# Kernel tuning notes

Hardware: AMD Instinct MI355X
Metric: run time of the kernel (lower is better)

## Reference

```python
import math
import jax, jax.numpy as jnp
import numpy as np

N = 100000       # nodes
K = 32           # fixed neighbor fanout
D_IN = 128
D_OUT = 128
TPERC = 0.45


def setup_inputs() -> dict:
    key = jax.random.key(0)
    k1, k2, k3 = jax.random.split(key, 3)
    x = jax.random.normal(k1, (N, D_IN), dtype=jnp.float32)
    # nn.Linear weight [out, in], no bias
    W = jax.random.normal(k2, (D_OUT, D_IN), dtype=jnp.float32) * (1.0 / math.sqrt(D_IN))
    nbrs = jax.random.randint(k3, (N, K), 0, N, dtype=jnp.int32)
    return {"x": x, "W": W, "nbrs": nbrs}


def reference(x, W, nbrs):
    # h = Linear(x): [N, D_OUT]
    h = jnp.einsum("nd,od->no", x, W)
    # gather neighbor messages: [N, K, D_OUT]
    msgs = h[nbrs]
    # per-channel sort over the neighbor axis (matches torch.sort(dim=0) per node)
    msgs = jnp.sort(msgs, axis=1)
    remove = math.floor(K * TPERC)  # static: 14
    if remove > 0:
        msgs = msgs[:, remove:K - remove]
    # trimmed mean over remaining neighbors; activation is identity (None)
    return jnp.mean(msgs, axis=1)
```

## Files before the change

kernel.cpp:

```cpp
#include <hip/hip_runtime.h>
#include <hip/hip_fp16.h>

#define NN 100000
#define KK 32
#define DD 128

typedef _Float16 v8h __attribute__((ext_vector_type(8)));
typedef _Float16 v4h __attribute__((ext_vector_type(4)));
typedef _Float16 v2h __attribute__((ext_vector_type(2)));
typedef float    v4f __attribute__((ext_vector_type(4)));

#define LDH 136

__global__ __launch_bounds__(256)
void gemm_mfma_kernel(const float* __restrict__ x, const float* __restrict__ W,
                      _Float16* __restrict__ h) {
    __shared__ _Float16 w_lds[DD * LDH];
    __shared__ _Float16 x_lds[128 * LDH];

    const int tid = threadIdx.x;
    const int block_row = blockIdx.x * 128;

    {
        const float4* ws = (const float4*)W;
        #pragma unroll
        for (int t = 0; t < 16; ++t) {
            const int fi = tid + 256 * t;
            const int r = fi >> 5, c4 = fi & 31;
            const float4 f = ws[fi];
            v4h p = { (_Float16)f.x, (_Float16)f.y, (_Float16)f.z, (_Float16)f.w };
            *(v4h*)&w_lds[r * LDH + c4 * 4] = p;
        }
    }
    {
        const float4* xs = (const float4*)x;
        #pragma unroll
        for (int t = 0; t < 16; ++t) {
            const int fi = tid + 256 * t;
            const int r = fi >> 5, c4 = fi & 31;
            const int gr = block_row + r;
            float4 f = make_float4(0.f, 0.f, 0.f, 0.f);
            if (gr < NN) f = xs[(size_t)gr * 32 + c4];
            v4h p = { (_Float16)f.x, (_Float16)f.y, (_Float16)f.z, (_Float16)f.w };
            *(v4h*)&x_lds[r * LDH + c4 * 4] = p;
        }
    }
    __syncthreads();

    const int wv   = tid >> 6;
    const int lane = tid & 63;
    const int m    = lane & 15;
    const int quad = lane >> 4;

    const v4f zero = {0.f, 0.f, 0.f, 0.f};
    v4f acc[2][8];
    #pragma unroll
    for (int nt = 0; nt < 2; ++nt)
        #pragma unroll
        for (int ot = 0; ot < 8; ++ot) acc[nt][ot] = zero;

    #pragma unroll
    for (int ks = 0; ks < 4; ++ks) {
        const int kb = ks * 32 + quad * 8;
        const v8h xf0 = *(const v8h*)&x_lds[(wv * 32 + m) * LDH + kb];
        const v8h xf1 = *(const v8h*)&x_lds[(wv * 32 + 16 + m) * LDH + kb];
        #pragma unroll
        for (int ot = 0; ot < 8; ++ot) {
            const v8h wf = *(const v8h*)&w_lds[(ot * 16 + m) * LDH + kb];
            acc[0][ot] = __builtin_amdgcn_mfma_f32_16x16x32_f16(wf, xf0, acc[0][ot], 0, 0, 0);
            acc[1][ot] = __builtin_amdgcn_mfma_f32_16x16x32_f16(wf, xf1, acc[1][ot], 0, 0, 0);
        }
    }

    #pragma unroll
    for (int nt = 0; nt < 2; ++nt) {
        const int xr = block_row + wv * 32 + nt * 16 + m;
        if (xr < NN) {
            #pragma unroll
            for (int ot = 0; ot < 8; ++ot) {
                const v4f a = acc[nt][ot];
                v4h p = { (_Float16)a.x, (_Float16)a.y, (_Float16)a.z, (_Float16)a.w };
                *(v4h*)&h[(size_t)xr * DD + ot * 16 + quad * 4] = p;
            }
        }
    }
}

struct CEp { signed char a, b; };
struct Net16 { CEp ce[63]; };

constexpr int oem_merge(CEp* out, int c, int lo, int n, int r) {
    const int m = r * 2;
    if (m < n) {
        c = oem_merge(out, c, lo, n, m);
        c = oem_merge(out, c, lo + r, n, m);
        for (int i = lo + r; i + r < lo + n; i += m) {
            out[c].a = (signed char)i; out[c].b = (signed char)(i + r); ++c;
        }
    } else {
        out[c].a = (signed char)lo; out[c].b = (signed char)(lo + r); ++c;
    }
    return c;
}
constexpr int oem_sort(CEp* out, int c, int lo, int n) {
    if (n > 1) {
        const int m = n / 2;
        c = oem_sort(out, c, lo, m);
        c = oem_sort(out, c, lo + m, m);
        c = oem_merge(out, c, lo, n, 1);
    }
    return c;
}
constexpr Net16 make_net16() {
    Net16 net{};
    (void)oem_sort(net.ce, 0, 0, 16);
    return net;
}
constexpr Net16 NET16 = make_net16();

constexpr int WMAP(int i) { return i < 16 ? i : 47 - i; }

#define PKMIN(d, s0, s1) asm("v_pk_min_f16 %0, %1, %2" : "=v"(d) : "v"(s0), "v"(s1))
#define PKMAX(d, s0, s1) asm("v_pk_max_f16 %0, %1, %2" : "=v"(d) : "v"(s0), "v"(s1))

#define CEW(p, q) do {                                                  \
    v2h na_, xa_, nb_, xb_;                                             \
    PKMIN(na_, va[p], va[q]); PKMAX(xa_, va[p], va[q]);                 \
    PKMIN(nb_, vb[p], vb[q]); PKMAX(xb_, vb[p], vb[q]);                 \
    va[p] = na_; va[q] = xa_; vb[p] = nb_; vb[q] = xb_; } while (0)

__global__ __launch_bounds__(256)
void trimmed_mean_kernel(const _Float16* __restrict__ h, const int* __restrict__ nbrs,
                         float* __restrict__ out) {
    __shared__ int s_nbr[8][KK];

    const int tid = threadIdx.x;
    const int row_base = blockIdx.x * 8;

    s_nbr[tid >> 5][tid & 31] = nbrs[(size_t)row_base * KK + tid];
    __syncthreads();

    const int brow = tid >> 5;
    const int cq   = tid & 31;
    const int row  = row_base + brow;

    const uint2* hq = (const uint2*)h;

    v2h va[KK];
    v2h vb[KK];
    #pragma unroll
    for (int k = 0; k < KK; ++k) {
        const int idx = s_nbr[brow][k];
        const uint2 u = hq[idx * 32 + cq];
        va[k] = __builtin_bit_cast(v2h, u.x);
        vb[k] = __builtin_bit_cast(v2h, u.y);
    }

    #pragma unroll
    for (int t = 0; t < 63; ++t) CEW(NET16.ce[t].a, NET16.ce[t].b);
    #pragma unroll
    for (int t = 0; t < 63; ++t) CEW(NET16.ce[t].a + 16, NET16.ce[t].b + 16);

    #pragma unroll
    for (int i = 0; i < 16; ++i) CEW(WMAP(i), WMAP(i + 16));
    #pragma unroll
    for (int i = 0; i < 8; ++i) { CEW(WMAP(i), WMAP(i + 8));
                                  CEW(WMAP(i + 16), WMAP(i + 24)); }
    #pragma unroll
    for (int i = 8; i < 12; ++i) { CEW(WMAP(i), WMAP(i + 4));
                                   CEW(WMAP(i + 8), WMAP(i + 12)); }
    CEW(WMAP(12), WMAP(14)); CEW(WMAP(13), WMAP(15));
    CEW(WMAP(16), WMAP(18)); CEW(WMAP(17), WMAP(19));

    float4 o;
    o.x = ((float)va[14].x + (float)va[15].x + (float)va[31].x + (float)va[30].x) * 0.25f;
    o.y = ((float)va[14].y + (float)va[15].y + (float)va[31].y + (float)va[30].y) * 0.25f;
    o.z = ((float)vb[14].x + (float)vb[15].x + (float)vb[31].x + (float)vb[30].x) * 0.25f;
    o.w = ((float)vb[14].y + (float)vb[15].y + (float)vb[31].y + (float)vb[30].y) * 0.25f;
    ((float4*)(out + (size_t)row * DD))[cq] = o;
}

extern "C" void kernel_launch(void* const* d_in, const int* in_sizes, int n_in,
                              void* d_out, int out_size, void* d_ws, size_t ws_size,
                              hipStream_t stream) {
    const float* x    = (const float*)d_in[0];
    const float* W    = (const float*)d_in[1];
    const int*   nbrs = (const int*)d_in[2];
    float*       out  = (float*)d_out;
    _Float16*    h    = (_Float16*)d_ws;

    (void)in_sizes; (void)n_in; (void)out_size; (void)ws_size;

    gemm_mfma_kernel<<<(NN + 127) / 128, 256, 0, stream>>>(x, W, h);
    trimmed_mean_kernel<<<NN / 8, 256, 0, stream>>>(h, nbrs, out);
}
```

Measured before the change: 228.6 us.

## Split h into column slices and process one slice per block

The GEMM now writes h in a sliced layout: four column slices of 32 fp16 each, stored as contiguous [NN,32] arrays. The trimmed-mean kernel assigns one slice per block, with 16 rows per block and 16 threads per row. Each thread loads one 32-bit fp16 pair per neighbor instead of two, which halves the register arrays. The aim is better cache locality for the random gathers, since each slice is a smaller working set, and higher occupancy from lower register pressure. The cost is that neighbor indices are loaded four times and there are more blocks with narrower 4-byte gathers.

```diff
diff --git a/kernel.cpp b/kernel.cpp
--- a/kernel.cpp
+++ b/kernel.cpp
@@ -11,6 +11,7 @@
 typedef float    v4f __attribute__((ext_vector_type(4)));
 
 #define LDH 136
+
 
 __global__ __launch_bounds__(256)
 void gemm_mfma_kernel(const float* __restrict__ x, const float* __restrict__ W,
@@ -80,7 +81,10 @@
             for (int ot = 0; ot < 8; ++ot) {
                 const v4f a = acc[nt][ot];
                 v4h p = { (_Float16)a.x, (_Float16)a.y, (_Float16)a.z, (_Float16)a.w };
-                *(v4h*)&h[(size_t)xr * DD + ot * 16 + quad * 4] = p;
+                const int c   = ot * 16 + quad * 4;
+                const int s   = c >> 5;
+                const int col = c & 31;
+                *(v4h*)&h[((size_t)s * NN + xr) * 32 + col] = p;
             }
         }
     }
@@ -124,36 +128,38 @@
 #define PKMAX(d, s0, s1) asm("v_pk_max_f16 %0, %1, %2" : "=v"(d) : "v"(s0), "v"(s1))
 
 #define CEW(p, q) do {                                                  \
-    v2h na_, xa_, nb_, xb_;                                             \
-    PKMIN(na_, va[p], va[q]); PKMAX(xa_, va[p], va[q]);                 \
-    PKMIN(nb_, vb[p], vb[q]); PKMAX(xb_, vb[p], vb[q]);                 \
-    va[p] = na_; va[q] = xa_; vb[p] = nb_; vb[q] = xb_; } while (0)
+    v2h n_, x_;                                                         \
+    PKMIN(n_, va[p], va[q]); PKMAX(x_, va[p], va[q]);                   \
+    va[p] = n_; va[q] = x_; } while (0)
 
 __global__ __launch_bounds__(256)
 void trimmed_mean_kernel(const _Float16* __restrict__ h, const int* __restrict__ nbrs,
                          float* __restrict__ out) {
-    __shared__ int s_nbr[8][KK];
-
-    const int tid = threadIdx.x;
-    const int row_base = blockIdx.x * 8;
-
-    s_nbr[tid >> 5][tid & 31] = nbrs[(size_t)row_base * KK + tid];
+    __shared__ int s_nbr[16][33];
+
+    const int tid      = threadIdx.x;
+    const int slice    = blockIdx.x & 3;
+    const int row_base = (blockIdx.x >> 2) * 16;
+
+    {
+        const int2 v = ((const int2*)(nbrs + (size_t)row_base * KK))[tid];
+        const int li = tid * 2;
+        const int r = li >> 5, c = li & 31;
+        s_nbr[r][c] = v.x; s_nbr[r][c + 1] = v.y;
+    }
     __syncthreads();
 
-    const int brow = tid >> 5;
-    const int cq   = tid & 31;
-    const int row  = row_base + brow;
-
-    const uint2* hq = (const uint2*)h;
+    const int q   = tid & 15;
+    const int r   = tid >> 4;
+    const int row = row_base + r;
+
+    const unsigned int* hs = (const unsigned int*)h + (size_t)slice * NN * 16;
 
     v2h va[KK];
-    v2h vb[KK];
     #pragma unroll
     for (int k = 0; k < KK; ++k) {
-        const int idx = s_nbr[brow][k];
-        const uint2 u = hq[idx * 32 + cq];
-        va[k] = __builtin_bit_cast(v2h, u.x);
-        vb[k] = __builtin_bit_cast(v2h, u.y);
+        const int idx = s_nbr[r][k];
+        va[k] = __builtin_bit_cast(v2h, hs[idx * 16 + q]);
     }
 
     #pragma unroll
@@ -172,12 +178,10 @@
     CEW(WMAP(12), WMAP(14)); CEW(WMAP(13), WMAP(15));
     CEW(WMAP(16), WMAP(18)); CEW(WMAP(17), WMAP(19));
 
-    float4 o;
+    float2 o;
     o.x = ((float)va[14].x + (float)va[15].x + (float)va[31].x + (float)va[30].x) * 0.25f;
     o.y = ((float)va[14].y + (float)va[15].y + (float)va[31].y + (float)va[30].y) * 0.25f;
-    o.z = ((float)vb[14].x + (float)vb[15].x + (float)vb[31].x + (float)vb[30].x) * 0.25f;
-    o.w = ((float)vb[14].y + (float)vb[15].y + (float)vb[31].y + (float)vb[30].y) * 0.25f;
-    ((float4*)(out + (size_t)row * DD))[cq] = o;
+    ((float2*)(out + (size_t)row * DD + slice * 32))[q] = o;
 }
 
 extern "C" void kernel_launch(void* const* d_in, const int* in_sizes, int n_in,
@@ -192,5 +196,5 @@
     (void)in_sizes; (void)n_in; (void)out_size; (void)ws_size;
 
     gemm_mfma_kernel<<<(NN + 127) / 128, 256, 0, stream>>>(x, W, h);
-    trimmed_mean_kernel<<<NN / 8, 256, 0, stream>>>(h, nbrs, out);
-}
+    trimmed_mean_kernel<<<(NN / 16) * 4, 256, 0, stream>>>(h, nbrs, out);
+}
```

New measurement: 220.9 us. 1.04x faster.
